# Kernel tuning notes

Hardware: AMD Instinct MI355X
Metric: run time of the kernel (lower is better)

Reference implementation:

```python
import jax, jax.numpy as jnp
import numpy as np

ALPHA = 0.2  # LeakyReLU negative slope
NEG_INF = -9e15  # mask value used by the original module


def setup_inputs() -> dict:
    key = jax.random.key(0)
    k1, k2, k3, k4 = jax.random.split(key, 4)
    B, N, F_in, F_out = 8, 2048, 128, 64
    h = jax.random.normal(k1, (B, N, F_in), dtype=jnp.float32)
    adj = jax.random.randint(k2, (B, N, N), 0, 2, dtype=jnp.int32)
    # xavier_uniform with gain=1.414
    def xavier(k, shape, gain=1.414):
        fan_in, fan_out = shape[0], shape[1]
        bound = gain * np.sqrt(6.0 / (fan_in + fan_out))
        return jax.random.uniform(k, shape, jnp.float32, -bound, bound)
    W = xavier(k3, (F_in, F_out))
    a = xavier(k4, (2 * F_out, 1))
    return {"h": h, "adj": adj, "W": W, "a": a}


def reference(h, adj, W, a):
    # h: [B,N,F_in], adj: [B,N,N], W: [F_in,F_out], a: [2*F_out,1]
    F_out = W.shape[1]
    Wh = jnp.matmul(h, W)                       # [B,N,F_out]
    # Rank-1 decomposition of the additive score: e_ij = leaky_relu(a1.Wh_i + a2.Wh_j)
    # (same math as cat([Wh_i, Wh_j]) @ a, without the O(N^2 * 2F) intermediate)
    a1 = a[:F_out, 0]
    a2 = a[F_out:, 0]
    s1 = jnp.einsum('bnf,f->bn', Wh, a1)        # scores for node i
    s2 = jnp.einsum('bnf,f->bn', Wh, a2)        # scores for node j
    e = jax.nn.leaky_relu(s1[:, :, None] + s2[:, None, :], negative_slope=ALPHA)  # [B,N,N]
    attention = jnp.where(adj > 0, e, jnp.float32(NEG_INF))
    attention = jax.nn.softmax(attention, axis=2)
    # dropout is identity in eval mode
    h_out = jnp.matmul(attention, Wh)           # [B,N,F_out]
    return jax.nn.elu(h_out), attention
```

## Files before the change

kernel.cpp:

```cpp
#include <hip/hip_runtime.h>

#define GAT_ALPHA 0.2f
#define INV_N (1.0f / 2048.0f)

typedef float f32x4 __attribute__((ext_vector_type(4)));
typedef __bf16 bf16x8 __attribute__((ext_vector_type(8)));
typedef unsigned short us8 __attribute__((ext_vector_type(8)));
typedef unsigned short us4 __attribute__((ext_vector_type(4)));

__device__ __forceinline__ unsigned short f2bf(float x) {
  union { float f; unsigned u; } v; v.f = x;
  unsigned r = v.u + 0x7FFFu + ((v.u >> 16) & 1u);
  return (unsigned short)(r >> 16);
}
__device__ __forceinline__ bf16x8 as_bf16(us8 u) {
  union { us8 a; bf16x8 b; } c; c.a = u; return c.b;
}
__device__ __forceinline__ float lrelu(float x) {
  return fmaxf(x, 0.f) + GAT_ALPHA * fminf(x, 0.f);
}
__device__ __forceinline__ void lgkm_barrier() {
  asm volatile("s_waitcnt lgkmcnt(0)" ::: "memory");
  __builtin_amdgcn_s_barrier();
  __builtin_amdgcn_sched_barrier(0);
}

__global__ __launch_bounds__(256)
void k0_wh(const float* __restrict__ h, const float* __restrict__ W,
           const float* __restrict__ a, unsigned short* __restrict__ WhT,
           float* __restrict__ s1g, float* __restrict__ s2g)
{
  __shared__ float h_s[64][132];
  __shared__ float W_s[128][64];
  __shared__ float wt_s[64][66];
  __shared__ float a_s[128];
  const int t = threadIdx.x;
  const int b = blockIdx.y;
  const int r0 = blockIdx.x * 64;

#pragma unroll
  for (int v = 0; v < 8; ++v) {
    int c = v * 256 + t;
    int k = c >> 4, fo = (c & 15) << 2;
    *(float4*)&W_s[k][fo] = *(const float4*)&W[k * 64 + fo];
  }
#pragma unroll
  for (int v = 0; v < 8; ++v) {
    int c = v * 256 + t;
    int r = c >> 5, ko = (c & 31) << 2;
    *(float4*)&h_s[r][ko] = *(const float4*)&h[((size_t)(b * 2048 + r0 + r)) * 128 + ko];
  }
  if (t < 128) a_s[t] = a[t];
  __syncthreads();

  const int tg = t >> 4;
  const int tf = (t & 15) << 2;
  float acc[4][4] = {};
#pragma unroll
  for (int k4 = 0; k4 < 32; ++k4) {
    float4 hv[4];
#pragma unroll
    for (int i = 0; i < 4; ++i)
      hv[i] = *(const float4*)&h_s[i * 16 + tg][k4 * 4];
#pragma unroll
    for (int kk = 0; kk < 4; ++kk) {
      float4 wv = *(const float4*)&W_s[k4 * 4 + kk][tf];
#pragma unroll
      for (int i = 0; i < 4; ++i) {
        float hx = ((const float*)&hv[i])[kk];
        acc[i][0] = fmaf(hx, wv.x, acc[i][0]);
        acc[i][1] = fmaf(hx, wv.y, acc[i][1]);
        acc[i][2] = fmaf(hx, wv.z, acc[i][2]);
        acc[i][3] = fmaf(hx, wv.w, acc[i][3]);
      }
    }
  }
#pragma unroll
  for (int i = 0; i < 4; ++i)
#pragma unroll
    for (int j = 0; j < 4; ++j)
      wt_s[tf + j][i * 16 + tg] = acc[i][j];
  __syncthreads();

  if (t < 64) {
    float v1 = 0.f, v2 = 0.f;
#pragma unroll 8
    for (int f = 0; f < 64; ++f) {
      float w = wt_s[f][t];
      v1 = fmaf(w, a_s[f], v1);
      v2 = fmaf(w, a_s[64 + f], v2);
    }
    s1g[b * 2048 + r0 + t] = v1;
    s2g[b * 2048 + r0 + t] = v2;
  }
  {
    int f = t >> 2, rb = (t & 3) << 4;
    unsigned short pk[16];
#pragma unroll
    for (int i = 0; i < 16; ++i) pk[i] = f2bf(wt_s[f][rb + i]);
    size_t base = ((size_t)(b * 64 + f)) * 2048 + r0 + rb;
    *(uint4*)&WhT[base]     = *(uint4*)&pk[0];
    *(uint4*)&WhT[base + 8] = *(uint4*)&pk[8];
  }
}

__global__ __launch_bounds__(256)
void k1_stats(const int* __restrict__ adj, const float* __restrict__ s1g,
              const float* __restrict__ s2g, float* __restrict__ mrow,
              float* __restrict__ lrow, unsigned long long* __restrict__ gmask)
{
  const int t = threadIdx.x;
  const int l = t & 63, w = t >> 6;
  const int b = blockIdx.y;
  const int i = blockIdx.x * 4 + w;
  const size_t row = (size_t)(b * 2048 + i);
  const int* __restrict__ arow = adj + row * 2048;
  const float* __restrict__ z = s2g + b * 2048;
  unsigned long long* __restrict__ g = gmask + row * 32;

  float4 zv[8];
  unsigned pb = 0;
  float M = -INFINITY;
#pragma unroll
  for (int c = 0; c < 8; ++c) {
    const int4 av = *(const int4*)&arow[c * 256 + 4 * l];
    zv[c] = *(const float4*)&z[c * 256 + 4 * l];
    const bool p0 = av.x > 0, p1 = av.y > 0, p2 = av.z > 0, p3 = av.w > 0;
    unsigned long long b0 = __ballot(p0), b1 = __ballot(p1);
    unsigned long long b2 = __ballot(p2), b3 = __ballot(p3);
    if (l == 0) {
      ulonglong2 u0; u0.x = b0; u0.y = b1;
      ulonglong2 u1; u1.x = b2; u1.y = b3;
      *(ulonglong2*)&g[c * 4]     = u0;
      *(ulonglong2*)&g[c * 4 + 2] = u1;
    }
    pb |= (unsigned(p0) | (unsigned(p1) << 1) | (unsigned(p2) << 2) | (unsigned(p3) << 3)) << (c * 4);
    M = fmaxf(M, p0 ? zv[c].x : -INFINITY);
    M = fmaxf(M, p1 ? zv[c].y : -INFINITY);
    M = fmaxf(M, p2 ? zv[c].z : -INFINITY);
    M = fmaxf(M, p3 ? zv[c].w : -INFINITY);
  }
#pragma unroll
  for (int o = 32; o > 0; o >>= 1) M = fmaxf(M, __shfl_xor(M, o));

  const float s1v = s1g[row];
  const float mv = lrelu(s1v + M);

  float sum = 0.f;
#pragma unroll
  for (int c = 0; c < 8; ++c) {
    sum += ((pb >> (c * 4)) & 1u) ? __expf(lrelu(s1v + zv[c].x) - mv) : 0.f;
    sum += ((pb >> (c * 4 + 1)) & 1u) ? __expf(lrelu(s1v + zv[c].y) - mv) : 0.f;
    sum += ((pb >> (c * 4 + 2)) & 1u) ? __expf(lrelu(s1v + zv[c].z) - mv) : 0.f;
    sum += ((pb >> (c * 4 + 3)) & 1u) ? __expf(lrelu(s1v + zv[c].w) - mv) : 0.f;
  }
#pragma unroll
  for (int o = 32; o > 0; o >>= 1) sum += __shfl_xor(sum, o);

  if (l == 0) {
    mrow[row] = mv;
    lrow[row] = sum;
  }
}

__global__ __launch_bounds__(256)
void k2_main(const unsigned long long* __restrict__ gmask,
             const unsigned short* __restrict__ WhT,
             const float* __restrict__ s1g, const float* __restrict__ s2g,
             const float* __restrict__ mrow, const float* __restrict__ lrow,
             float* __restrict__ pp0, float* __restrict__ pp1,
             float* __restrict__ att)
{
  __shared__ unsigned short att_s[32][136];
  __shared__ unsigned short wh_s[64][136];
  __shared__ unsigned long long bm_s[32][16];
  __shared__ float s1_s[32], m_s[32], il_s[32];

  const int t = threadIdx.x;
  const int b = blockIdx.z;
  const int jh = blockIdx.y;
  const int jb = jh << 10;
  const int r0 = blockIdx.x * 32;
  const size_t rowb = (size_t)(b * 2048 + r0);

  {
    int rr = t >> 3, wq = (t & 7) << 1;
    ulonglong2 v = *(const ulonglong2*)&gmask[(rowb + rr) * 32 + jh * 16 + wq];
    bm_s[rr][wq] = v.x; bm_s[rr][wq + 1] = v.y;
  }
  if (t < 32) {
    float L = lrow[rowb + t];
    s1_s[t] = s1g[rowb + t];
    m_s[t]  = mrow[rowb + t];
    il_s[t] = (L > 0.f) ? 1.f / L : -1.f;
  }
  __syncthreads();

  const int w  = t >> 6, l = t & 63;
  const int rt  = (w & 1) << 4;
  const int ft0 = (w >> 1) << 1;
  const int ln = l & 15, lg = l >> 4;
  f32x4 acc0 = {0.f, 0.f, 0.f, 0.f};
  f32x4 acc1 = {0.f, 0.f, 0.f, 0.f};

  const int ff = t >> 4, ko = (t & 15) << 3;

  for (int j0 = jb; j0 < jb + 1024; j0 += 128) {
    uint4 wreg[4];
#pragma unroll
    for (int v = 0; v < 4; ++v)
      wreg[v] = *(const uint4*)&WhT[((size_t)(b * 64 + (v * 16 + ff))) * 2048 + j0 + ko];

#pragma unroll
    for (int it = 0; it < 4; ++it) {
      const int r  = (t >> 5) + (it << 3);
      const int jj = (t & 31) << 2;
      const int j  = j0 + jj;
      const float s1v = s1_s[r], mv = m_s[r], il = il_s[r];
      const bool uni = (il < 0.f);
      const int lc4 = ((j >> 8) & 3) << 2;
      const int pos = (j & 255) >> 2;
      const unsigned long long w0 = bm_s[r][lc4 + 0];
      const unsigned long long w1 = bm_s[r][lc4 + 1];
      const unsigned long long w2 = bm_s[r][lc4 + 2];
      const unsigned long long w3 = bm_s[r][lc4 + 3];
      const float4 zv = *(const float4*)&s2g[b * 2048 + j];
      float4 o;
      {
        float e = __expf(lrelu(s1v + zv.x) - mv) * il;
        o.x = uni ? INV_N : ((((w0 >> pos) & 1ull) != 0) ? e : 0.f);
      }
      {
        float e = __expf(lrelu(s1v + zv.y) - mv) * il;
        o.y = uni ? INV_N : ((((w1 >> pos) & 1ull) != 0) ? e : 0.f);
      }
      {
        float e = __expf(lrelu(s1v + zv.z) - mv) * il;
        o.z = uni ? INV_N : ((((w2 >> pos) & 1ull) != 0) ? e : 0.f);
      }
      {
        float e = __expf(lrelu(s1v + zv.w) - mv) * il;
        o.w = uni ? INV_N : ((((w3 >> pos) & 1ull) != 0) ? e : 0.f);
      }
      *(float4*)&att[(rowb + r) * 2048 + j] = o;
      us4 pk;
      pk.x = f2bf(o.x); pk.y = f2bf(o.y); pk.z = f2bf(o.z); pk.w = f2bf(o.w);
      *(us4*)&att_s[r][jj] = pk;
    }
#pragma unroll
    for (int v = 0; v < 4; ++v)
      *(uint4*)&wh_s[v * 16 + ff][ko] = wreg[v];

    lgkm_barrier();
#pragma unroll
    for (int ks = 0; ks < 4; ++ks) {
      bf16x8 af  = as_bf16(*(const us8*)&att_s[rt + ln][ks * 32 + lg * 8]);
      bf16x8 bf0 = as_bf16(*(const us8*)&wh_s[ft0 * 16 + ln][ks * 32 + lg * 8]);
      bf16x8 bf1 = as_bf16(*(const us8*)&wh_s[ft0 * 16 + 16 + ln][ks * 32 + lg * 8]);
      acc0 = __builtin_amdgcn_mfma_f32_16x16x32_bf16(af, bf0, acc0, 0, 0, 0);
      acc1 = __builtin_amdgcn_mfma_f32_16x16x32_bf16(af, bf1, acc1, 0, 0, 0);
    }
    lgkm_barrier();
  }
  float* __restrict__ pp = (jh == 0) ? pp0 : pp1;
#pragma unroll
  for (int q = 0; q < 4; ++q) {
    int r = rt + lg * 4 + q;
    pp[(rowb + r) * 64 + ft0 * 16 + ln]       = acc0[q];
    pp[(rowb + r) * 64 + (ft0 + 1) * 16 + ln] = acc1[q];
  }
}

__global__ __launch_bounds__(256)
void k3_elu(const float* __restrict__ pp0, const float* __restrict__ pp1,
            float* __restrict__ hout)
{
  const size_t idx = ((size_t)blockIdx.x * 256 + threadIdx.x) * 4;
  float4 a = *(const float4*)&pp0[idx];
  float4 c = *(const float4*)&pp1[idx];
  float4 o;
  float x;
  x = a.x + c.x; o.x = (x > 0.f) ? x : expm1f(x);
  x = a.y + c.y; o.y = (x > 0.f) ? x : expm1f(x);
  x = a.z + c.z; o.z = (x > 0.f) ? x : expm1f(x);
  x = a.w + c.w; o.w = (x > 0.f) ? x : expm1f(x);
  *(float4*)&hout[idx] = o;
}

extern "C" void kernel_launch(void* const* d_in, const int* in_sizes, int n_in,
                              void* d_out, int out_size, void* d_ws, size_t ws_size,
                              hipStream_t stream)
{
  const float* h   = (const float*)d_in[0];
  const int*   adj = (const int*)d_in[1];
  const float* W   = (const float*)d_in[2];
  const float* a   = (const float*)d_in[3];
  float* hout = (float*)d_out;
  float* att  = hout + (size_t)8 * 2048 * 64;

  char* ws = (char*)d_ws;
  unsigned short* WhT = (unsigned short*)ws;
  float* s1 = (float*)(ws + (size_t)(2u << 20));
  float* s2 = s1 + 16384;
  float* mr = s2 + 16384;
  float* lr = mr + 16384;
  unsigned long long* gmask =
      (unsigned long long*)(ws + (size_t)(2u << 20) + 4 * 65536);
  float* pp0 = (float*)(ws + (size_t)(2u << 20) + 4 * 65536 + (4u << 20));
  float* pp1 = pp0 + (size_t)8 * 2048 * 64;

  k0_wh   <<<dim3(32, 8),     256, 0, stream>>>(h, W, a, WhT, s1, s2);
  k1_stats<<<dim3(512, 8),    256, 0, stream>>>(adj, s1, s2, mr, lr, gmask);
  k2_main <<<dim3(64, 2, 8),  256, 0, stream>>>(gmask, WhT, s1, s2, mr, lr, pp0, pp1, att);
  k3_elu  <<<dim3(1024),      256, 0, stream>>>(pp0, pp1, hout);
}
```

Before: 81.27 us.

## Fuse stats, attention and aggregation kernels into one per-row-block kernel

Merges the row-statistics, attention/MFMA aggregation and ELU kernels into a single kernel. Each block handles 16 rows over the full column range, so it no longer needs the global bitmask, partial-sum buffers or a separate ELU pass. The adjacency mask is kept as 16-bit words in shared memory, and s2 is staged in LDS. The softmax max-subtraction is dropped: exponentials are taken directly and normalized by their sum, which assumes scores stay in a safe range. Adjacency loads and attention stores use nontemporal hints.

```diff
diff --git a/kernel.cpp b/kernel.cpp
--- a/kernel.cpp
+++ b/kernel.cpp
@@ -4,9 +4,9 @@
 #define INV_N (1.0f / 2048.0f)
 
 typedef float f32x4 __attribute__((ext_vector_type(4)));
+typedef int   i32x4 __attribute__((ext_vector_type(4)));
 typedef __bf16 bf16x8 __attribute__((ext_vector_type(8)));
 typedef unsigned short us8 __attribute__((ext_vector_type(8)));
-typedef unsigned short us4 __attribute__((ext_vector_type(4)));
 
 __device__ __forceinline__ unsigned short f2bf(float x) {
   union { float f; unsigned u; } v; v.f = x;
@@ -104,148 +104,93 @@
   }
 }
 
-__global__ __launch_bounds__(256)
-void k1_stats(const int* __restrict__ adj, const float* __restrict__ s1g,
-              const float* __restrict__ s2g, float* __restrict__ mrow,
-              float* __restrict__ lrow, unsigned long long* __restrict__ gmask)
+__global__ __launch_bounds__(256, 4)
+void k12_main(const int* __restrict__ adj, const unsigned short* __restrict__ WhT,
+              const float* __restrict__ s1g, const float* __restrict__ s2g,
+              float* __restrict__ hout, float* __restrict__ att)
 {
+  __shared__ float z_s[2048];
+  __shared__ unsigned short mask_s[16][128];
+  __shared__ unsigned short wh_s[64][136];
+  __shared__ unsigned short att_s[16][136];
+
   const int t = threadIdx.x;
-  const int l = t & 63, w = t >> 6;
   const int b = blockIdx.y;
-  const int i = blockIdx.x * 4 + w;
-  const size_t row = (size_t)(b * 2048 + i);
-  const int* __restrict__ arow = adj + row * 2048;
-  const float* __restrict__ z = s2g + b * 2048;
-  unsigned long long* __restrict__ g = gmask + row * 32;
-
-  float4 zv[8];
-  unsigned pb = 0;
-  float M = -INFINITY;
+  const int r0 = blockIdx.x * 16;
+  const size_t rowb = (size_t)(b * 2048 + r0);
+  const int r = t >> 4;
+  const int q = t & 15;
+
+  *(float4*)&z_s[t * 8]     = *(const float4*)&s2g[b * 2048 + t * 8];
+  *(float4*)&z_s[t * 8 + 4] = *(const float4*)&s2g[b * 2048 + t * 8 + 4];
+  __syncthreads();
+
+  const float s1v = s1g[rowb + r];
+  const int* __restrict__ arow = adj + (rowb + r) * 2048;
+
+  float sum = 0.f;
 #pragma unroll
   for (int c = 0; c < 8; ++c) {
-    const int4 av = *(const int4*)&arow[c * 256 + 4 * l];
-    zv[c] = *(const float4*)&z[c * 256 + 4 * l];
-    const bool p0 = av.x > 0, p1 = av.y > 0, p2 = av.z > 0, p3 = av.w > 0;
-    unsigned long long b0 = __ballot(p0), b1 = __ballot(p1);
-    unsigned long long b2 = __ballot(p2), b3 = __ballot(p3);
-    if (l == 0) {
-      ulonglong2 u0; u0.x = b0; u0.y = b1;
-      ulonglong2 u1; u1.x = b2; u1.y = b3;
-      *(ulonglong2*)&g[c * 4]     = u0;
-      *(ulonglong2*)&g[c * 4 + 2] = u1;
-    }
-    pb |= (unsigned(p0) | (unsigned(p1) << 1) | (unsigned(p2) << 2) | (unsigned(p3) << 3)) << (c * 4);
-    M = fmaxf(M, p0 ? zv[c].x : -INFINITY);
-    M = fmaxf(M, p1 ? zv[c].y : -INFINITY);
-    M = fmaxf(M, p2 ? zv[c].z : -INFINITY);
-    M = fmaxf(M, p3 ? zv[c].w : -INFINITY);
-  }
-#pragma unroll
-  for (int o = 32; o > 0; o >>= 1) M = fmaxf(M, __shfl_xor(M, o));
-
-  const float s1v = s1g[row];
-  const float mv = lrelu(s1v + M);
-
-  float sum = 0.f;
-#pragma unroll
-  for (int c = 0; c < 8; ++c) {
-    sum += ((pb >> (c * 4)) & 1u) ? __expf(lrelu(s1v + zv[c].x) - mv) : 0.f;
-    sum += ((pb >> (c * 4 + 1)) & 1u) ? __expf(lrelu(s1v + zv[c].y) - mv) : 0.f;
-    sum += ((pb >> (c * 4 + 2)) & 1u) ? __expf(lrelu(s1v + zv[c].z) - mv) : 0.f;
-    sum += ((pb >> (c * 4 + 3)) & 1u) ? __expf(lrelu(s1v + zv[c].w) - mv) : 0.f;
-  }
-#pragma unroll
-  for (int o = 32; o > 0; o >>= 1) sum += __shfl_xor(sum, o);
-
-  if (l == 0) {
-    mrow[row] = mv;
-    lrow[row] = sum;
-  }
-}
-
-__global__ __launch_bounds__(256)
-void k2_main(const unsigned long long* __restrict__ gmask,
-             const unsigned short* __restrict__ WhT,
-             const float* __restrict__ s1g, const float* __restrict__ s2g,
-             const float* __restrict__ mrow, const float* __restrict__ lrow,
-             float* __restrict__ pp0, float* __restrict__ pp1,
-             float* __restrict__ att)
-{
-  __shared__ unsigned short att_s[32][136];
-  __shared__ unsigned short wh_s[64][136];
-  __shared__ unsigned long long bm_s[32][16];
-  __shared__ float s1_s[32], m_s[32], il_s[32];
-
-  const int t = threadIdx.x;
-  const int b = blockIdx.z;
-  const int jh = blockIdx.y;
-  const int jb = jh << 10;
-  const int r0 = blockIdx.x * 32;
-  const size_t rowb = (size_t)(b * 2048 + r0);
-
-  {
-    int rr = t >> 3, wq = (t & 7) << 1;
-    ulonglong2 v = *(const ulonglong2*)&gmask[(rowb + rr) * 32 + jh * 16 + wq];
-    bm_s[rr][wq] = v.x; bm_s[rr][wq + 1] = v.y;
-  }
-  if (t < 32) {
-    float L = lrow[rowb + t];
-    s1_s[t] = s1g[rowb + t];
-    m_s[t]  = mrow[rowb + t];
-    il_s[t] = (L > 0.f) ? 1.f / L : -1.f;
-  }
+    const int jb = c * 256 + q * 16;
+    i32x4 a0 = __builtin_nontemporal_load((const i32x4*)&arow[jb]);
+    i32x4 a1 = __builtin_nontemporal_load((const i32x4*)&arow[jb + 4]);
+    i32x4 a2 = __builtin_nontemporal_load((const i32x4*)&arow[jb + 8]);
+    i32x4 a3 = __builtin_nontemporal_load((const i32x4*)&arow[jb + 12]);
+    const float4 z0 = *(const float4*)&z_s[jb];
+    const float4 z1 = *(const float4*)&z_s[jb + 4];
+    const float4 z2 = *(const float4*)&z_s[jb + 8];
+    const float4 z3 = *(const float4*)&z_s[jb + 12];
+    unsigned bits = 0;
+#define P1(av, zz, k)                                            \
+    { bool p = (av) > 0;                                         \
+      bits |= (unsigned)p << (k);                                \
+      sum += p ? __expf(lrelu(s1v + (zz))) : 0.f; }
+    P1(a0.x, z0.x, 0)  P1(a0.y, z0.y, 1)  P1(a0.z, z0.z, 2)  P1(a0.w, z0.w, 3)
+    P1(a1.x, z1.x, 4)  P1(a1.y, z1.y, 5)  P1(a1.z, z1.z, 6)  P1(a1.w, z1.w, 7)
+    P1(a2.x, z2.x, 8)  P1(a2.y, z2.y, 9)  P1(a2.z, z2.z, 10) P1(a2.w, z2.w, 11)
+    P1(a3.x, z3.x, 12) P1(a3.y, z3.y, 13) P1(a3.z, z3.z, 14) P1(a3.w, z3.w, 15)
+#undef P1
+    mask_s[r][c * 16 + q] = (unsigned short)bits;
+  }
+#pragma unroll
+  for (int o = 1; o < 16; o <<= 1) sum += __shfl_xor(sum, o);
+  const float il = (sum > 0.f) ? 1.f / sum : -1.f;
+  const bool uni = (il < 0.f);
   __syncthreads();
 
   const int w  = t >> 6, l = t & 63;
-  const int rt  = (w & 1) << 4;
-  const int ft0 = (w >> 1) << 1;
   const int ln = l & 15, lg = l >> 4;
-  f32x4 acc0 = {0.f, 0.f, 0.f, 0.f};
-  f32x4 acc1 = {0.f, 0.f, 0.f, 0.f};
-
-  const int ff = t >> 4, ko = (t & 15) << 3;
-
-  for (int j0 = jb; j0 < jb + 1024; j0 += 128) {
+  const int ff = t >> 4, ko = q * 8;
+  f32x4 acc = {0.f, 0.f, 0.f, 0.f};
+
+  for (int j0 = 0; j0 < 2048; j0 += 128) {
     uint4 wreg[4];
 #pragma unroll
     for (int v = 0; v < 4; ++v)
-      wreg[v] = *(const uint4*)&WhT[((size_t)(b * 64 + (v * 16 + ff))) * 2048 + j0 + ko];
-
-#pragma unroll
-    for (int it = 0; it < 4; ++it) {
-      const int r  = (t >> 5) + (it << 3);
-      const int jj = (t & 31) << 2;
-      const int j  = j0 + jj;
-      const float s1v = s1_s[r], mv = m_s[r], il = il_s[r];
-      const bool uni = (il < 0.f);
-      const int lc4 = ((j >> 8) & 3) << 2;
-      const int pos = (j & 255) >> 2;
-      const unsigned long long w0 = bm_s[r][lc4 + 0];
-      const unsigned long long w1 = bm_s[r][lc4 + 1];
-      const unsigned long long w2 = bm_s[r][lc4 + 2];
-      const unsigned long long w3 = bm_s[r][lc4 + 3];
-      const float4 zv = *(const float4*)&s2g[b * 2048 + j];
-      float4 o;
-      {
-        float e = __expf(lrelu(s1v + zv.x) - mv) * il;
-        o.x = uni ? INV_N : ((((w0 >> pos) & 1ull) != 0) ? e : 0.f);
-      }
-      {
-        float e = __expf(lrelu(s1v + zv.y) - mv) * il;
-        o.y = uni ? INV_N : ((((w1 >> pos) & 1ull) != 0) ? e : 0.f);
-      }
-      {
-        float e = __expf(lrelu(s1v + zv.z) - mv) * il;
-        o.z = uni ? INV_N : ((((w2 >> pos) & 1ull) != 0) ? e : 0.f);
-      }
-      {
-        float e = __expf(lrelu(s1v + zv.w) - mv) * il;
-        o.w = uni ? INV_N : ((((w3 >> pos) & 1ull) != 0) ? e : 0.f);
-      }
-      *(float4*)&att[(rowb + r) * 2048 + j] = o;
-      us4 pk;
-      pk.x = f2bf(o.x); pk.y = f2bf(o.y); pk.z = f2bf(o.z); pk.w = f2bf(o.w);
-      *(us4*)&att_s[r][jj] = pk;
+      wreg[v] = *(const uint4*)&WhT[((size_t)(b * 64 + v * 16 + ff)) * 2048 + j0 + ko];
+
+    const int j = j0 + q * 8;
+    unsigned mb = mask_s[r][j >> 4];
+    mb >>= (j & 8);
+    const float4 za = *(const float4*)&z_s[j];
+    const float4 zb = *(const float4*)&z_s[j + 4];
+    float4 oa, ob;
+#define P2(dst, zz, k)                                             \
+    { float e = __expf(lrelu(s1v + (zz))) * il;                    \
+      dst = uni ? INV_N : (((mb >> (k)) & 1u) ? e : 0.f); }
+    P2(oa.x, za.x, 0) P2(oa.y, za.y, 1) P2(oa.z, za.z, 2) P2(oa.w, za.w, 3)
+    P2(ob.x, zb.x, 4) P2(ob.y, zb.y, 5) P2(ob.z, zb.z, 6) P2(ob.w, zb.w, 7)
+#undef P2
+    {
+      union { float4 f; f32x4 v; } ua, ub; ua.f = oa; ub.f = ob;
+      __builtin_nontemporal_store(ua.v, (f32x4*)&att[(rowb + r) * 2048 + j]);
+      __builtin_nontemporal_store(ub.v, (f32x4*)&att[(rowb + r) * 2048 + j + 4]);
+    }
+    {
+      us8 pk;
+      pk[0] = f2bf(oa.x); pk[1] = f2bf(oa.y); pk[2] = f2bf(oa.z); pk[3] = f2bf(oa.w);
+      pk[4] = f2bf(ob.x); pk[5] = f2bf(ob.y); pk[6] = f2bf(ob.z); pk[7] = f2bf(ob.w);
+      *(us8*)&att_s[r][q * 8] = pk;
     }
 #pragma unroll
     for (int v = 0; v < 4; ++v)
@@ -254,37 +199,19 @@
     lgkm_barrier();
 #pragma unroll
     for (int ks = 0; ks < 4; ++ks) {
-      bf16x8 af  = as_bf16(*(const us8*)&att_s[rt + ln][ks * 32 + lg * 8]);
-      bf16x8 bf0 = as_bf16(*(const us8*)&wh_s[ft0 * 16 + ln][ks * 32 + lg * 8]);
-      bf16x8 bf1 = as_bf16(*(const us8*)&wh_s[ft0 * 16 + 16 + ln][ks * 32 + lg * 8]);
-      acc0 = __builtin_amdgcn_mfma_f32_16x16x32_bf16(af, bf0, acc0, 0, 0, 0);
-      acc1 = __builtin_amdgcn_mfma_f32_16x16x32_bf16(af, bf1, acc1, 0, 0, 0);
+      bf16x8 af = as_bf16(*(const us8*)&att_s[ln][ks * 32 + lg * 8]);
+      bf16x8 bf = as_bf16(*(const us8*)&wh_s[w * 16 + ln][ks * 32 + lg * 8]);
+      acc = __builtin_amdgcn_mfma_f32_16x16x32_bf16(af, bf, acc, 0, 0, 0);
     }
     lgkm_barrier();
   }
-  float* __restrict__ pp = (jh == 0) ? pp0 : pp1;
-#pragma unroll
-  for (int q = 0; q < 4; ++q) {
-    int r = rt + lg * 4 + q;
-    pp[(rowb + r) * 64 + ft0 * 16 + ln]       = acc0[q];
-    pp[(rowb + r) * 64 + (ft0 + 1) * 16 + ln] = acc1[q];
-  }
-}
-
-__global__ __launch_bounds__(256)
-void k3_elu(const float* __restrict__ pp0, const float* __restrict__ pp1,
-            float* __restrict__ hout)
-{
-  const size_t idx = ((size_t)blockIdx.x * 256 + threadIdx.x) * 4;
-  float4 a = *(const float4*)&pp0[idx];
-  float4 c = *(const float4*)&pp1[idx];
-  float4 o;
-  float x;
-  x = a.x + c.x; o.x = (x > 0.f) ? x : expm1f(x);
-  x = a.y + c.y; o.y = (x > 0.f) ? x : expm1f(x);
-  x = a.z + c.z; o.z = (x > 0.f) ? x : expm1f(x);
-  x = a.w + c.w; o.w = (x > 0.f) ? x : expm1f(x);
-  *(float4*)&hout[idx] = o;
+
+#pragma unroll
+  for (int q4 = 0; q4 < 4; ++q4) {
+    const int rr = lg * 4 + q4;
+    const float x = acc[q4];
+    hout[(rowb + rr) * 64 + w * 16 + ln] = (x > 0.f) ? x : expm1f(x);
+  }
 }
 
 extern "C" void kernel_launch(void* const* d_in, const int* in_sizes, int n_in,
@@ -302,15 +229,7 @@
   unsigned short* WhT = (unsigned short*)ws;
   float* s1 = (float*)(ws + (size_t)(2u << 20));
   float* s2 = s1 + 16384;
-  float* mr = s2 + 16384;
-  float* lr = mr + 16384;
-  unsigned long long* gmask =
-      (unsigned long long*)(ws + (size_t)(2u << 20) + 4 * 65536);
-  float* pp0 = (float*)(ws + (size_t)(2u << 20) + 4 * 65536 + (4u << 20));
-  float* pp1 = pp0 + (size_t)8 * 2048 * 64;
-
-  k0_wh   <<<dim3(32, 8),     256, 0, stream>>>(h, W, a, WhT, s1, s2);
-  k1_stats<<<dim3(512, 8),    256, 0, stream>>>(adj, s1, s2, mr, lr, gmask);
-  k2_main <<<dim3(64, 2, 8),  256, 0, stream>>>(gmask, WhT, s1, s2, mr, lr, pp0, pp1, att);
-  k3_elu  <<<dim3(1024),      256, 0, stream>>>(pp0, pp1, hout);
-}
+
+  k0_wh   <<<dim3(32, 8),  256, 0, stream>>>(h, W, a, WhT, s1, s2);
+  k12_main<<<dim3(128, 8), 256, 0, stream>>>(adj, WhT, s1, s2, hout, att);
+}
```

Measured after the change: 101.0 us. +24.3%, slower.
